# Kernel tuning notes

Hardware: AMD Instinct MI355X
Metric: run time of the kernel (lower is better)

The kernel has to match this reference:

```python
import math
import jax, jax.numpy as jnp
import numpy as np

VOCAB, D, H, L, DFF, MAXLEN, PAD = 32000, 512, 8, 6, 2048, 5000, 0
DK = D // H
EPS = 1e-5


def _positional_encoding(max_len, d_model):
    pos = np.arange(max_len, dtype=np.float32)[:, None]
    div = np.exp(np.arange(0, d_model, 2, dtype=np.float32) * (-math.log(10000.0) / d_model))
    pe = np.zeros((max_len, d_model), dtype=np.float32)
    pe[:, 0::2] = np.sin(pos * div)
    pe[:, 1::2] = np.cos(pos * div)
    return jnp.asarray(pe)


def setup_inputs() -> dict:
    key = jax.random.key(0)
    ks = jax.random.split(key, 16)
    B, S = 2, 2048
    src = jax.random.randint(ks[0], (B, S), 0, VOCAB)
    emb = jax.random.normal(ks[1], (VOCAB, D), jnp.float32) * (D ** -0.5)
    emb = emb.at[PAD].set(0.0)  # padding_idx row zeroed
    pe = _positional_encoding(MAXLEN, D)
    s = 0.02
    WQ = jax.random.normal(ks[2], (L, D, D), jnp.float32) * s
    WK = jax.random.normal(ks[3], (L, D, D), jnp.float32) * s
    WV = jax.random.normal(ks[4], (L, D, D), jnp.float32) * s
    WO = jax.random.normal(ks[5], (L, D, D), jnp.float32) * s
    W1 = jax.random.normal(ks[6], (L, D, DFF), jnp.float32) * s
    b1 = jnp.zeros((L, DFF), jnp.float32)
    W2 = jax.random.normal(ks[7], (L, DFF, D), jnp.float32) * s
    b2 = jnp.zeros((L, D), jnp.float32)
    ln1_s = jnp.ones((L, D), jnp.float32); ln1_b = jnp.zeros((L, D), jnp.float32)
    ln2_s = jnp.ones((L, D), jnp.float32); ln2_b = jnp.zeros((L, D), jnp.float32)
    fn_s = jnp.ones((D,), jnp.float32); fn_b = jnp.zeros((D,), jnp.float32)
    return dict(src=src, emb=emb, pe=pe, WQ=WQ, WK=WK, WV=WV, WO=WO,
                W1=W1, b1=b1, W2=W2, b2=b2, ln1_s=ln1_s, ln1_b=ln1_b,
                ln2_s=ln2_s, ln2_b=ln2_b, fn_s=fn_s, fn_b=fn_b)


def _layernorm(x, scale, bias):
    mu = jnp.mean(x, axis=-1, keepdims=True)
    var = jnp.mean(jnp.square(x - mu), axis=-1, keepdims=True)
    return (x - mu) * jax.lax.rsqrt(var + EPS) * scale + bias


def _encoder_forward(src, emb, pe, WQ, WK, WV, WO, W1, b1, W2, b2,
                     ln1_s, ln1_b, ln2_s, ln2_b, fn_s, fn_b):
    B, S = src.shape
    key_mask = (src != PAD)[:, None, None, :]  # [B,1,1,S] padding mask
    x = emb[src] * math.sqrt(D) + pe[:S]        # [B,S,D] (dropout=eval/off)
    for l in range(L):
        # --- pre-LN self-attention ---
        h = _layernorm(x, ln1_s[l], ln1_b[l])
        q = (h @ WQ[l]).reshape(B, S, H, DK).transpose(0, 2, 1, 3)
        k = (h @ WK[l]).reshape(B, S, H, DK).transpose(0, 2, 1, 3)
        v = (h @ WV[l]).reshape(B, S, H, DK).transpose(0, 2, 1, 3)
        scores = jnp.einsum('bhqd,bhkd->bhqk', q, k) / math.sqrt(DK)
        scores = jnp.where(key_mask, scores, -jnp.inf)
        w = jax.nn.softmax(scores, axis=-1)
        w = jnp.nan_to_num(w, nan=0.0)
        attn = jnp.einsum('bhqk,bhkd->bhqd', w, v)
        attn = attn.transpose(0, 2, 1, 3).reshape(B, S, D) @ WO[l]
        x = x + attn
        # --- pre-LN FFN ---
        h = _layernorm(x, ln2_s[l], ln2_b[l])
        h = jax.nn.relu(h @ W1[l] + b1[l]) @ W2[l] + b2[l]
        x = x + h
    return _layernorm(x, fn_s, fn_b)


def reference(src, emb, pe, WQ, WK, WV, WO, W1, b1, W2, b2,
              ln1_s, ln1_b, ln2_s, ln2_b, fn_s, fn_b):
    return _encoder_forward(src, emb, pe, WQ, WK, WV, WO, W1, b1, W2, b2,
                            ln1_s, ln1_b, ln2_s, ln2_b, fn_s, fn_b)
```

## Files before the change

kernel.cpp:

```cpp
#include <hip/hip_runtime.h>


typedef _Float16 f16;
typedef _Float16 f16x8 __attribute__((ext_vector_type(8)));
typedef _Float16 f16x4 __attribute__((ext_vector_type(4)));
typedef float    f32x4 __attribute__((ext_vector_type(4)));

#define MFMA16(a, b, c) __builtin_amdgcn_mfma_f32_16x16x32_f16((a), (b), (c), 0, 0, 0)
#define GLOAD_LDS16(GP, LP)                                        \
  __builtin_amdgcn_global_load_lds(                                \
      (const __attribute__((address_space(1))) void*)(GP),         \
      (__attribute__((address_space(3))) void*)(LP), 16, 0, 0)

__device__ inline float fast_exp2(float x) {
#if __has_builtin(__builtin_amdgcn_exp2f)
  return __builtin_amdgcn_exp2f(x);
#else
  return exp2f(x);
#endif
}

static constexpr int Dm  = 512;
static constexpr int Sx  = 2048;
static constexpr int NTOK = 4096;
static constexpr int DFFm = 2048;
static constexpr int Lc  = 6;

__global__ __launch_bounds__(256) void transpose_all(
    const float* __restrict__ WQ, const float* __restrict__ WK,
    const float* __restrict__ WV, const float* __restrict__ WO,
    const float* __restrict__ W1, const float* __restrict__ W2,
    f16* __restrict__ wqkv, f16* __restrict__ wtO,
    f16* __restrict__ wt1, f16* __restrict__ wt2)
{
  __shared__ float t[32][33];
  const size_t DD = (size_t)Dm * Dm;
  const size_t DQKV = (size_t)1536 * Dm;
  const size_t DF = (size_t)Dm * DFFm;
  int id = blockIdx.x;
  const float* src; f16* dst; int R, C, bx, by;
  if (id < 6144) {
    const int z = id >> 8, rem = id & 255;
    bx = rem & 15; by = rem >> 4;
    const int widx = z / 6, layer = z % 6;
    src = ((widx == 0) ? WQ : (widx == 1) ? WK : (widx == 2) ? WV : WO)
          + (size_t)layer * DD;
    dst = (widx < 3) ? wqkv + (size_t)layer * DQKV + (size_t)widx * 512 * Dm
                     : wtO + (size_t)layer * DD;
    R = 512; C = 512;
  } else if (id < 12288) {
    id -= 6144;
    const int layer = id >> 10, rem = id & 1023;
    bx = rem & 63; by = rem >> 6;
    src = W1 + (size_t)layer * DF;
    dst = wt1 + (size_t)layer * DF;
    R = 512; C = 2048;
  } else {
    id -= 12288;
    const int layer = id >> 10, rem = id & 1023;
    bx = rem & 15; by = rem >> 4;
    src = W2 + (size_t)layer * DF;
    dst = wt2 + (size_t)layer * DF;
    R = 2048; C = 512;
  }
  const int r0 = by * 32, c0 = bx * 32;
  const int tx = threadIdx.x, ty = threadIdx.y;
  #pragma unroll
  for (int i = 0; i < 4; i++)
    t[ty + i * 8][tx] = src[(size_t)(r0 + ty + i * 8) * C + c0 + tx];
  __syncthreads();
  #pragma unroll
  for (int i = 0; i < 4; i++)
    dst[(size_t)(c0 + ty + i * 8) * R + r0 + tx] = (f16)t[tx][ty + i * 8];
}

__global__ __launch_bounds__(256) void embed_k(
    const int* __restrict__ src, const float* __restrict__ emb,
    const float* __restrict__ pe, f16* __restrict__ x, float* __restrict__ mb)
{
  const int gid = blockIdx.x * 256 + threadIdx.x;
  const int token = gid >> 6;
  const int d0 = (gid & 63) << 3;
  const int s = token & (Sx - 1);
  const int tk = src[token];
  if ((gid & 63) == 0) mb[token] = (tk != 0) ? 0.f : -3.0e38f;
  const float* e = emb + (size_t)tk * Dm + d0;
  const float* p = pe + (size_t)s * Dm + d0;
  const float SC = 22.627416997969522f;
  f16x8 o;
  #pragma unroll
  for (int j = 0; j < 8; j++) o[j] = (f16)(e[j] * SC + p[j]);
  *(f16x8*)(x + (size_t)token * Dm + d0) = o;
}

template <typename OUT, int ADD, int BIAS, int WRITEX>
__global__ __launch_bounds__(256) void lnf_k(
    const f16* __restrict__ x, const f16* __restrict__ part,
    const f16* __restrict__ part2, const float* __restrict__ bias,
    const float* __restrict__ sc, const float* __restrict__ bi,
    OUT* __restrict__ out, f16* __restrict__ xout)
{
  const int row = blockIdx.x * 4 + (threadIdx.x >> 6);
  const int l = threadIdx.x & 63;
  f16x8 xv = *(const f16x8*)(x + (size_t)row * Dm + l * 8);
  float v[8];
  #pragma unroll
  for (int j = 0; j < 8; j++) v[j] = (float)xv[j];
  if constexpr (ADD >= 1) {
    f16x8 p = *(const f16x8*)(part + (size_t)row * Dm + l * 8);
    #pragma unroll
    for (int j = 0; j < 8; j++) v[j] += (float)p[j];
    if constexpr (ADD == 2) {
      f16x8 p2 = *(const f16x8*)(part2 + (size_t)row * Dm + l * 8);
      #pragma unroll
      for (int j = 0; j < 8; j++) v[j] += (float)p2[j];
    }
    if constexpr (BIAS) {
      float bb[8];
      *(float4*)&bb[0] = *(const float4*)(bias + l * 8);
      *(float4*)&bb[4] = *(const float4*)(bias + l * 8 + 4);
      #pragma unroll
      for (int j = 0; j < 8; j++) v[j] += bb[j];
    }
    if constexpr (WRITEX) {
      f16x8 xo;
      #pragma unroll
      for (int j = 0; j < 8; j++) xo[j] = (f16)v[j];
      *(f16x8*)(xout + (size_t)row * Dm + l * 8) = xo;
    }
  }
  float s = 0.f;
  #pragma unroll
  for (int j = 0; j < 8; j++) s += v[j];
  #pragma unroll
  for (int m = 1; m < 64; m <<= 1) s += __shfl_xor(s, m);
  const float mu = s * (1.0f / 512.0f);
  float qv = 0.f;
  #pragma unroll
  for (int j = 0; j < 8; j++) { float d = v[j] - mu; qv += d * d; }
  #pragma unroll
  for (int m = 1; m < 64; m <<= 1) qv += __shfl_xor(qv, m);
  const float inv = rsqrtf(qv * (1.0f / 512.0f) + 1e-5f);
  float scv[8], biv[8];
  *(float4*)&scv[0] = *(const float4*)(sc + l * 8);
  *(float4*)&scv[4] = *(const float4*)(sc + l * 8 + 4);
  *(float4*)&biv[0] = *(const float4*)(bi + l * 8);
  *(float4*)&biv[4] = *(const float4*)(bi + l * 8 + 4);
  if constexpr (sizeof(OUT) == 2) {
    f16x8 o;
    #pragma unroll
    for (int j = 0; j < 8; j++) o[j] = (f16)((v[j] - mu) * inv * scv[j] + biv[j]);
    *(f16x8*)((f16*)out + (size_t)row * Dm + l * 8) = o;
  } else {
    float o[8];
    #pragma unroll
    for (int j = 0; j < 8; j++) o[j] = (v[j] - mu) * inv * scv[j] + biv[j];
    float* po = (float*)out + (size_t)row * Dm + l * 8;
    *(float4*)po = *(float4*)&o[0];
    *(float4*)(po + 4) = *(float4*)&o[4];
  }
}

template <int BN, int MODE, int N, int K, int SK>
__global__ __launch_bounds__(256) void gemm_k(
    const f16* __restrict__ A, const f16* __restrict__ Bt,
    f16* __restrict__ O0, f16* __restrict__ O1, f16* __restrict__ O2,
    const float* __restrict__ bias)
{
  constexpr int BM = 128;
  constexpr int NF = (BN >= 32) ? BN / 32 : 1;
  constexpr int NBM = NTOK / BM;
  constexpr int NBN = N / BN;
  constexpr int NB = NBM * NBN * SK;
  __shared__ f16 lsA[2][BM * 64];
  __shared__ f16 lsB[2][BN * 64];
  const int tid = threadIdx.x;
  const int l = tid & 63, w = tid >> 6;
  const int lr = l & 15, lh = l >> 4;
  const int wm = w >> 1, wn = w & 1;
  const int bid = blockIdx.x;
  const int nid = (bid & 7) * (NB / 8) + (bid >> 3);
  const int ks = nid / (NBM * NBN);
  const int rr = nid % (NBM * NBN);
  const int bm = rr / NBN, bn = rr % NBN;

  constexpr int ACH = (BM * 64) / (256 * 8);
  constexpr int BCH = (BN * 64) / (256 * 8);
  const size_t rowA0 = (size_t)bm * BM;
  const size_t rowB0 = (size_t)bn * BN;
  const int k0 = ks * (K / SK);

  auto stage = [&](int kt, int pb) {
    #pragma unroll
    for (int i = 0; i < ACH; i++) {
      int c = i * 256 + tid, r = c >> 3, g = c & 7, gs = g ^ (r & 7);
      GLOAD_LDS16(A + (rowA0 + r) * K + k0 + kt * 64 + gs * 8, &lsA[pb][c * 8]);
    }
    #pragma unroll
    for (int i = 0; i < BCH; i++) {
      int c = i * 256 + tid, r = c >> 3, g = c & 7, gs = g ^ (r & 7);
      GLOAD_LDS16(Bt + (rowB0 + r) * K + k0 + kt * 64 + gs * 8, &lsB[pb][c * 8]);
    }
  };

  f32x4 acc[4][NF] = {};
  stage(0, 0);
  constexpr int NT = (K / SK) >> 6;
  for (int kt = 0; kt < NT; ++kt) {
    const int cur = kt & 1;
    __syncthreads();
    if (kt + 1 < NT) stage(kt + 1, cur ^ 1);
    #pragma unroll
    for (int s = 0; s < 2; s++) {
      const int gg = (s * 4 + lh) ^ (lr & 7);
      f16x8 af[4], bf[NF];
      #pragma unroll
      for (int mf = 0; mf < 4; mf++)
        af[mf] = *(const f16x8*)(&lsA[cur][(wm * 64 + mf * 16 + lr) * 64 + gg * 8]);
      #pragma unroll
      for (int nf = 0; nf < NF; nf++)
        bf[nf] = *(const f16x8*)(&lsB[cur][(wn * (BN / 2) + nf * 16 + lr) * 64 + gg * 8]);
      #pragma unroll
      for (int mf = 0; mf < 4; mf++)
        #pragma unroll
        for (int nf = 0; nf < NF; nf++)
          acc[mf][nf] = MFMA16(af[mf], bf[nf], acc[mf][nf]);
    }
  }

  #pragma unroll
  for (int mf = 0; mf < 4; mf++) {
    #pragma unroll
    for (int nf = 0; nf < NF; nf++) {
      const int token = bm * BM + wm * 64 + mf * 16 + lh * 4;
      const int ch = bn * BN + wn * (BN / 2) + nf * 16 + lr;
      if constexpr (MODE == 0) {
        const int part = ch >> 9;
        const int pch = ch & 511;
        if (part == 2) {
          f16x4 o;
          #pragma unroll
          for (int r = 0; r < 4; r++) o[r] = (f16)acc[mf][nf][r];
          const int bb = token >> 11, ss = token & (Sx - 1);
          const int scol = (ss & ~31) | (((ss >> 2) & 3) << 3) | (((ss >> 4) & 1) << 2);
          *(f16x4*)(O2 + ((size_t)((bb << 3) + (pch >> 6)) * 64 + (pch & 63)) * Sx + scol) = o;
        } else {
          f16* Oz = (part == 0) ? O0 : O1;
          #pragma unroll
          for (int r = 0; r < 4; r++)
            Oz[(size_t)(token + r) * Dm + pch] = (f16)acc[mf][nf][r];
        }
      } else if constexpr (MODE == 1) {
        #pragma unroll
        for (int r = 0; r < 4; r++)
          O0[(size_t)(token + r) * N + ch] = (f16)acc[mf][nf][r];
      } else if constexpr (MODE == 2) {
        #pragma unroll
        for (int r = 0; r < 4; r++) {
          float v = acc[mf][nf][r] + bias[ch];
          O0[(size_t)(token + r) * N + ch] = (f16)fmaxf(v, 0.f);
        }
      } else {
        f16* dst = O0 + (size_t)ks * NTOK * N;
        #pragma unroll
        for (int r = 0; r < 4; r++)
          dst[(size_t)(token + r) * N + ch] = (f16)acc[mf][nf][r];
      }
    }
  }
}

__global__ __launch_bounds__(512) void attn_k(
    const f16* __restrict__ q, const f16* __restrict__ kk,
    const f16* __restrict__ vt, const float* __restrict__ maskb,
    f16* __restrict__ out)
{
  __shared__ f16 lsK[2][2][64 * 64];
  __shared__ f16 lsV[2][2][64 * 64];
  const int tid = threadIdx.x;
  const int l = tid & 63, w = tid >> 6;
  const int lr = l & 15, lh = l >> 4;
  const int grp = w >> 2;
  const int t256 = tid & 255;
  const int bid = blockIdx.x;
  const int nid = ((bid & 7) << 6) + (bid >> 3);
  const int bh = nid >> 5;
  const int qt = nid & 31;
  const int b = bh >> 3, h = bh & 7;

  const _Float16 QS = (_Float16)0.18033688f;
  f16x8 qf[2];
  #pragma unroll
  for (int s = 0; s < 2; s++) {
    size_t row = (size_t)(b * Sx + qt * 64 + (w & 3) * 16 + lr);
    f16x8 t = *(const f16x8*)(q + row * Dm + h * 64 + s * 32 + lh * 8);
    qf[s] = t * QS;
  }

  const f16x8 ones = {(f16)1, (f16)1, (f16)1, (f16)1,
                      (f16)1, (f16)1, (f16)1, (f16)1};
  f32x4 oacc[4] = {};
  f32x4 sumacc = {};
  float mrun = -1e30f;

  auto stage = [&](int t, int pb) {
    #pragma unroll
    for (int i = 0; i < 2; i++) {
      int c = i * 256 + t256, r = c >> 3, g = c & 7, gs = g ^ (r & 7);
      GLOAD_LDS16(kk + (size_t)(b * Sx + t * 64 + r) * Dm + h * 64 + gs * 8,
                  &lsK[grp][pb][c * 8]);
      GLOAD_LDS16(vt + (size_t)(bh * 64 + r) * Sx + t * 64 + gs * 8,
                  &lsV[grp][pb][c * 8]);
    }
  };
  stage(grp * 16, 0);

  for (int i = 0; i < 16; ++i) {
    const int t = grp * 16 + i;
    const int cur = i & 1;
    __syncthreads();
    if (i < 15) stage(t + 1, cur ^ 1);

    f32x4 sacc[4];
    #pragma unroll
    for (int kf = 0; kf < 4; kf++)
      sacc[kf] = *(const f32x4*)(maskb + b * Sx + t * 64 + kf * 16 + lh * 4);
    __builtin_amdgcn_s_setprio(1);
    #pragma unroll
    for (int s = 0; s < 2; s++) {
      const int gk = (s * 4 + lh) ^ (lr & 7);
      #pragma unroll
      for (int kf = 0; kf < 4; kf++) {
        f16x8 a = *(const f16x8*)(&lsK[grp][cur][(kf * 16 + lr) * 64 + gk * 8]);
        sacc[kf] = MFMA16(a, qf[s], sacc[kf]);
      }
    }
    __builtin_amdgcn_s_setprio(0);

    float pmax;
    {
      float t0 = fmaxf(fmaxf(sacc[0][0], sacc[0][1]), sacc[0][2]);
      float t1 = fmaxf(fmaxf(sacc[0][3], sacc[1][0]), sacc[1][1]);
      float t2 = fmaxf(fmaxf(sacc[1][2], sacc[1][3]), sacc[2][0]);
      float t3 = fmaxf(fmaxf(sacc[2][1], sacc[2][2]), sacc[2][3]);
      float t4 = fmaxf(fmaxf(sacc[3][0], sacc[3][1]), sacc[3][2]);
      float u0 = fmaxf(fmaxf(t0, t1), sacc[3][3]);
      float u1 = fmaxf(fmaxf(t2, t3), t4);
      pmax = fmaxf(u0, u1);
    }
    pmax = fmaxf(pmax, __shfl_xor(pmax, 16));
    pmax = fmaxf(pmax, __shfl_xor(pmax, 32));
    if (!__all(pmax - mrun <= 8.0f)) {
      const float mnew = fmaxf(mrun, pmax);
      const float rs = fast_exp2(mrun - mnew);
      sumacc *= rs;
      #pragma unroll
      for (int mf = 0; mf < 4; mf++) oacc[mf] *= rs;
      mrun = mnew;
    }
    #pragma unroll
    for (int kf = 0; kf < 4; kf++)
      #pragma unroll
      for (int r = 0; r < 4; r++)
        sacc[kf][r] = fast_exp2(sacc[kf][r] - mrun);
    f16x8 pa[2];
    #pragma unroll
    for (int s = 0; s < 2; s++)
      #pragma unroll
      for (int jj = 0; jj < 8; jj++)
        pa[s][jj] = (f16)sacc[2 * s + (jj >> 2)][jj & 3];
    sumacc = MFMA16(ones, pa[0], sumacc);
    sumacc = MFMA16(ones, pa[1], sumacc);

    __builtin_amdgcn_s_setprio(1);
    #pragma unroll
    for (int s = 0; s < 2; s++) {
      const int gv = (4 * s + lh) ^ (lr & 7);
      #pragma unroll
      for (int mf = 0; mf < 4; mf++) {
        f16x8 vv = *(const f16x8*)(&lsV[grp][cur][(mf * 16 + lr) * 64 + gv * 8]);
        oacc[mf] = MFMA16(vv, pa[s], oacc[mf]);
      }
    }
    __builtin_amdgcn_s_setprio(0);
  }

  const float lrun = sumacc[0];
  __syncthreads();
  float* sO  = (float*)&lsK[0][0][0];
  float* sML = (float*)&lsV[0][0][0];
  const int wl = (w & 3) * 64 + l;
  if (grp == 1) {
    #pragma unroll
    for (int mf = 0; mf < 4; mf++)
      #pragma unroll
      for (int r = 0; r < 4; r++) sO[wl * 16 + mf * 4 + r] = oacc[mf][r];
    sML[wl * 2] = mrun;
    sML[wl * 2 + 1] = lrun;
  }
  __syncthreads();
  if (grp == 0) {
    const float m1 = sML[wl * 2], l1 = sML[wl * 2 + 1];
    const float mm = fmaxf(mrun, m1);
    const float s0 = fast_exp2(mrun - mm), s1 = fast_exp2(m1 - mm);
    const float inv = 1.f / (lrun * s0 + l1 * s1);
    size_t row = (size_t)(b * Sx + qt * 64 + (w & 3) * 16 + lr);
    #pragma unroll
    for (int mf = 0; mf < 4; mf++) {
      f16x4 o;
      #pragma unroll
      for (int r = 0; r < 4; r++)
        o[r] = (f16)((oacc[mf][r] * s0 + sO[wl * 16 + mf * 4 + r] * s1) * inv);
      *(f16x4*)(out + row * Dm + h * 64 + mf * 16 + lh * 4) = o;
    }
  }
}

extern "C" void kernel_launch(void* const* d_in, const int* in_sizes, int n_in,
                              void* d_out, int out_size, void* d_ws, size_t ws_size,
                              hipStream_t stream)
{
  (void)in_sizes; (void)n_in; (void)out_size; (void)ws_size;
  const int*   src  = (const int*)d_in[0];
  const float* emb  = (const float*)d_in[1];
  const float* pe   = (const float*)d_in[2];
  const float* WQ   = (const float*)d_in[3];
  const float* WK   = (const float*)d_in[4];
  const float* WV   = (const float*)d_in[5];
  const float* WO   = (const float*)d_in[6];
  const float* W1   = (const float*)d_in[7];
  const float* b1   = (const float*)d_in[8];
  const float* W2   = (const float*)d_in[9];
  const float* b2   = (const float*)d_in[10];
  const float* ln1s = (const float*)d_in[11];
  const float* ln1b = (const float*)d_in[12];
  const float* ln2s = (const float*)d_in[13];
  const float* ln2b = (const float*)d_in[14];
  const float* fns  = (const float*)d_in[15];
  const float* fnb  = (const float*)d_in[16];

  char* ws = (char*)d_ws;
  const size_t DD = (size_t)Dm * Dm;
  const size_t DQKV = (size_t)1536 * Dm;
  const size_t DF = (size_t)Dm * DFFm;
  f16* wqkv = (f16*)(ws);
  f16* wtO  = wqkv + Lc * DQKV;
  f16* wt1  = wtO + Lc * DD;
  f16* wt2  = wt1 + Lc * DF;
  f16* x    = wt2 + Lc * DF;
  f16* hbuf = x + (size_t)NTOK * Dm;
  f16* qb   = hbuf + (size_t)NTOK * Dm;
  f16* kb   = qb + (size_t)NTOK * Dm;
  f16* vtb  = kb + (size_t)NTOK * Dm;
  f16* attn = vtb + (size_t)NTOK * Dm;
  f16* aout = attn + (size_t)NTOK * Dm;
  f16* ff   = aout + (size_t)NTOK * Dm;
  f16* ffo  = ff + (size_t)NTOK * DFFm;
  float* maskb = (float*)(ffo + (size_t)2 * NTOK * Dm);

  transpose_all<<<18432, dim3(32, 8), 0, stream>>>(
      WQ, WK, WV, WO, W1, W2, wqkv, wtO, wt1, wt2);
  embed_k<<<1024, 256, 0, stream>>>(src, emb, pe, x, maskb);

  f16* ffo1 = ffo + (size_t)NTOK * Dm;
  for (int l = 0; l < Lc; l++) {
    const f16* wqkv_l = wqkv + (size_t)l * DQKV;
    const f16* wo = wtO + (size_t)l * DD;
    const f16* w1 = wt1 + (size_t)l * DF;
    const f16* w2 = wt2 + (size_t)l * DF;

    if (l == 0)
      lnf_k<f16, 0, 0, 0><<<1024, 256, 0, stream>>>(
          x, nullptr, nullptr, nullptr, ln1s, ln1b, hbuf, nullptr);
    else
      lnf_k<f16, 2, 1, 1><<<1024, 256, 0, stream>>>(
          x, ffo, ffo1, b2 + (size_t)(l - 1) * Dm, ln1s + l * Dm, ln1b + l * Dm,
          hbuf, x);
    gemm_k<64, 0, 1536, 512, 1><<<768, 256, 0, stream>>>(
        hbuf, wqkv_l, qb, kb, vtb, nullptr);
    attn_k<<<512, 512, 0, stream>>>(qb, kb, vtb, maskb, attn);
    gemm_k<32, 1, 512, 512, 1><<<512, 256, 0, stream>>>(
        attn, wo, aout, nullptr, nullptr, nullptr);
    lnf_k<f16, 1, 0, 1><<<1024, 256, 0, stream>>>(
        x, aout, nullptr, nullptr, ln2s + l * Dm, ln2b + l * Dm, hbuf, x);
    gemm_k<128, 2, 2048, 512, 1><<<512, 256, 0, stream>>>(
        hbuf, w1, ff, nullptr, nullptr, b1 + (size_t)l * DFFm);
    gemm_k<64, 3, 512, 2048, 2><<<512, 256, 0, stream>>>(
        ff, w2, ffo, nullptr, nullptr, nullptr);
  }

  lnf_k<float, 2, 1, 0><<<1024, 256, 0, stream>>>(
      x, ffo, ffo1, b2 + (size_t)(Lc - 1) * Dm, fns, fnb, (float*)d_out, nullptr);
}
```

Baseline: 600.1 us.

## Switch attention to 32x32 MFMA with four-way KV split per block

Rewrites the attention kernel to use 32x32x16 MFMA tiles instead of 16x16x32. Each block now runs four KV-split groups of two waves over 32-key tiles, where it used to run two groups of four waves over 64-key tiles. The row sum is now taken with a shuffle reduction instead of a ones-MFMA. The V-transpose write layout in the QKV projection epilogue is changed to match the new fragment ordering. The intent is fewer MFMA issues and more KV parallelism, in exchange for a four-way merge in LDS at the end and smaller tiles per iteration.

Result: slower. 637.1 us (+6.2%).

```diff
diff --git a/kernel.cpp b/kernel.cpp
--- a/kernel.cpp
+++ b/kernel.cpp
@@ -5,8 +5,10 @@
 typedef _Float16 f16x8 __attribute__((ext_vector_type(8)));
 typedef _Float16 f16x4 __attribute__((ext_vector_type(4)));
 typedef float    f32x4 __attribute__((ext_vector_type(4)));
+typedef float    f32x16 __attribute__((ext_vector_type(16)));
 
 #define MFMA16(a, b, c) __builtin_amdgcn_mfma_f32_16x16x32_f16((a), (b), (c), 0, 0, 0)
+#define MFMA32(a, b, c) __builtin_amdgcn_mfma_f32_32x32x16_f16((a), (b), (c), 0, 0, 0)
 #define GLOAD_LDS16(GP, LP)                                        \
   __builtin_amdgcn_global_load_lds(                                \
       (const __attribute__((address_space(1))) void*)(GP),         \
@@ -242,7 +244,8 @@
           #pragma unroll
           for (int r = 0; r < 4; r++) o[r] = (f16)acc[mf][nf][r];
           const int bb = token >> 11, ss = token & (Sx - 1);
-          const int scol = (ss & ~31) | (((ss >> 2) & 3) << 3) | (((ss >> 4) & 1) << 2);
+          const int scol = (ss & ~15) | (((ss >> 2) & 1) << 3)
+                         | (((ss >> 3) & 1) << 2) | (ss & 3);
           *(f16x4*)(O2 + ((size_t)((bb << 3) + (pch >> 6)) * 64 + (pch & 63)) * Sx + scol) = o;
         } else {
           f16* Oz = (part == 0) ? O0 : O1;
@@ -275,13 +278,14 @@
     const f16* __restrict__ vt, const float* __restrict__ maskb,
     f16* __restrict__ out)
 {
-  __shared__ f16 lsK[2][2][64 * 64];
-  __shared__ f16 lsV[2][2][64 * 64];
+  __shared__ f16 lds[32768];
+  f16* lsK = lds;
+  f16* lsV = lds + 16384;
   const int tid = threadIdx.x;
   const int l = tid & 63, w = tid >> 6;
-  const int lr = l & 15, lh = l >> 4;
-  const int grp = w >> 2;
-  const int t256 = tid & 255;
+  const int lq = l & 31, hi = l >> 5;
+  const int grp = w >> 1, wq = w & 1;
+  const int t128 = tid & 127;
   const int bid = blockIdx.x;
   const int nid = ((bid & 7) << 6) + (bid >> 3);
   const int bh = nid >> 5;
@@ -289,28 +293,34 @@
   const int b = bh >> 3, h = bh & 7;
 
   const _Float16 QS = (_Float16)0.18033688f;
-  f16x8 qf[2];
-  #pragma unroll
-  for (int s = 0; s < 2; s++) {
-    size_t row = (size_t)(b * Sx + qt * 64 + (w & 3) * 16 + lr);
-    f16x8 t = *(const f16x8*)(q + row * Dm + h * 64 + s * 32 + lh * 8);
-    qf[s] = t * QS;
-  }
-
-  const f16x8 ones = {(f16)1, (f16)1, (f16)1, (f16)1,
-                      (f16)1, (f16)1, (f16)1, (f16)1};
-  f32x4 oacc[4] = {};
-  f32x4 sumacc = {};
+  const size_t qrow = (size_t)(b * Sx + qt * 64 + wq * 32 + lq);
+  f16x8 qf[4];
+  #pragma unroll
+  for (int ks = 0; ks < 4; ks++) {
+    f16x8 t = *(const f16x8*)(q + qrow * Dm + h * 64 + ks * 16 + hi * 8);
+    qf[ks] = t * QS;
+  }
+
+  f32x16 oacc[2] = {};
   float mrun = -1e30f;
+  float lrun = 0.f;
 
   auto stage = [&](int t, int pb) {
+    f16* dK = lsK + (grp * 2 + pb) * 2048;
+    f16* dV = lsV + (grp * 2 + pb) * 2048;
     #pragma unroll
     for (int i = 0; i < 2; i++) {
-      int c = i * 256 + t256, r = c >> 3, g = c & 7, gs = g ^ (r & 7);
-      GLOAD_LDS16(kk + (size_t)(b * Sx + t * 64 + r) * Dm + h * 64 + gs * 8,
-                  &lsK[grp][pb][c * 8]);
-      GLOAD_LDS16(vt + (size_t)(bh * 64 + r) * Sx + t * 64 + gs * 8,
-                  &lsV[grp][pb][c * 8]);
+      int c = i * 128 + t128;
+      {
+        int r = c >> 3, g = c & 7, gs = g ^ (r & 7);
+        GLOAD_LDS16(kk + (size_t)(b * Sx + t * 32 + r) * Dm + h * 64 + gs * 8,
+                    dK + c * 8);
+      }
+      {
+        int dv = c >> 2, q2 = (c & 3) ^ (dv & 3);
+        GLOAD_LDS16(vt + (size_t)(bh * 64 + dv) * Sx + t * 32 + (q2 >> 1) * 16 + (q2 & 1) * 8,
+                    dV + c * 8);
+      }
     }
   };
   stage(grp * 16, 0);
@@ -320,99 +330,113 @@
     const int cur = i & 1;
     __syncthreads();
     if (i < 15) stage(t + 1, cur ^ 1);
-
-    f32x4 sacc[4];
-    #pragma unroll
-    for (int kf = 0; kf < 4; kf++)
-      sacc[kf] = *(const f32x4*)(maskb + b * Sx + t * 64 + kf * 16 + lh * 4);
+    const f16* cK = lsK + (grp * 2 + cur) * 2048;
+    const f16* cV = lsV + (grp * 2 + cur) * 2048;
+
+    f32x16 sacc;
+    #pragma unroll
+    for (int a = 0; a < 4; a++)
+      ((f32x4*)&sacc)[a] = *(const f32x4*)(maskb + b * Sx + t * 32 + 4 * hi + 8 * a);
     __builtin_amdgcn_s_setprio(1);
     #pragma unroll
-    for (int s = 0; s < 2; s++) {
-      const int gk = (s * 4 + lh) ^ (lr & 7);
-      #pragma unroll
-      for (int kf = 0; kf < 4; kf++) {
-        f16x8 a = *(const f16x8*)(&lsK[grp][cur][(kf * 16 + lr) * 64 + gk * 8]);
-        sacc[kf] = MFMA16(a, qf[s], sacc[kf]);
-      }
+    for (int ks = 0; ks < 4; ks++) {
+      f16x8 kf = *(const f16x8*)(cK + lq * 64 + (((ks * 2 + hi) ^ (lq & 7)) * 8));
+      sacc = MFMA32(kf, qf[ks], sacc);
     }
     __builtin_amdgcn_s_setprio(0);
 
     float pmax;
     {
-      float t0 = fmaxf(fmaxf(sacc[0][0], sacc[0][1]), sacc[0][2]);
-      float t1 = fmaxf(fmaxf(sacc[0][3], sacc[1][0]), sacc[1][1]);
-      float t2 = fmaxf(fmaxf(sacc[1][2], sacc[1][3]), sacc[2][0]);
-      float t3 = fmaxf(fmaxf(sacc[2][1], sacc[2][2]), sacc[2][3]);
-      float t4 = fmaxf(fmaxf(sacc[3][0], sacc[3][1]), sacc[3][2]);
-      float u0 = fmaxf(fmaxf(t0, t1), sacc[3][3]);
-      float u1 = fmaxf(fmaxf(t2, t3), t4);
-      pmax = fmaxf(u0, u1);
-    }
-    pmax = fmaxf(pmax, __shfl_xor(pmax, 16));
+      float t0 = fmaxf(fmaxf(sacc[0], sacc[1]), sacc[2]);
+      float t1 = fmaxf(fmaxf(sacc[3], sacc[4]), sacc[5]);
+      float t2 = fmaxf(fmaxf(sacc[6], sacc[7]), sacc[8]);
+      float t3 = fmaxf(fmaxf(sacc[9], sacc[10]), sacc[11]);
+      float t4 = fmaxf(fmaxf(sacc[12], sacc[13]), sacc[14]);
+      pmax = fmaxf(fmaxf(fmaxf(t0, t1), fmaxf(t2, t3)), fmaxf(t4, sacc[15]));
+    }
     pmax = fmaxf(pmax, __shfl_xor(pmax, 32));
     if (!__all(pmax - mrun <= 8.0f)) {
       const float mnew = fmaxf(mrun, pmax);
       const float rs = fast_exp2(mrun - mnew);
-      sumacc *= rs;
-      #pragma unroll
-      for (int mf = 0; mf < 4; mf++) oacc[mf] *= rs;
+      lrun *= rs;
+      oacc[0] *= rs;
+      oacc[1] *= rs;
       mrun = mnew;
     }
-    #pragma unroll
-    for (int kf = 0; kf < 4; kf++)
-      #pragma unroll
-      for (int r = 0; r < 4; r++)
-        sacc[kf][r] = fast_exp2(sacc[kf][r] - mrun);
-    f16x8 pa[2];
-    #pragma unroll
-    for (int s = 0; s < 2; s++)
-      #pragma unroll
-      for (int jj = 0; jj < 8; jj++)
-        pa[s][jj] = (f16)sacc[2 * s + (jj >> 2)][jj & 3];
-    sumacc = MFMA16(ones, pa[0], sumacc);
-    sumacc = MFMA16(ones, pa[1], sumacc);
+    float ps = 0.f;
+    #pragma unroll
+    for (int r = 0; r < 16; r++) {
+      float p = fast_exp2(sacc[r] - mrun);
+      sacc[r] = p;
+      ps += p;
+    }
+    ps += __shfl_xor(ps, 32);
+    lrun += ps;
+    f16x8 pb[2];
+    #pragma unroll
+    for (int g = 0; g < 2; g++)
+      #pragma unroll
+      for (int j = 0; j < 8; j++)
+        pb[g][j] = (f16)sacc[g * 8 + j];
 
     __builtin_amdgcn_s_setprio(1);
     #pragma unroll
-    for (int s = 0; s < 2; s++) {
-      const int gv = (4 * s + lh) ^ (lr & 7);
-      #pragma unroll
-      for (int mf = 0; mf < 4; mf++) {
-        f16x8 vv = *(const f16x8*)(&lsV[grp][cur][(mf * 16 + lr) * 64 + gv * 8]);
-        oacc[mf] = MFMA16(vv, pa[s], oacc[mf]);
+    for (int g = 0; g < 2; g++)
+      #pragma unroll
+      for (int mfv = 0; mfv < 2; mfv++) {
+        const int f = (mfv * 32 + lq) * 4 + ((2 * g + hi) ^ (lq & 3));
+        f16x8 vv = *(const f16x8*)(cV + f * 8);
+        oacc[mfv] = MFMA32(vv, pb[g], oacc[mfv]);
       }
-    }
     __builtin_amdgcn_s_setprio(0);
   }
 
-  const float lrun = sumacc[0];
   __syncthreads();
-  float* sO  = (float*)&lsK[0][0][0];
-  float* sML = (float*)&lsV[0][0][0];
-  const int wl = (w & 3) * 64 + l;
-  if (grp == 1) {
-    #pragma unroll
-    for (int mf = 0; mf < 4; mf++)
-      #pragma unroll
-      for (int r = 0; r < 4; r++) sO[wl * 16 + mf * 4 + r] = oacc[mf][r];
-    sML[wl * 2] = mrun;
-    sML[wl * 2 + 1] = lrun;
+  float* sO  = (float*)lds;
+  float* sML = (float*)lds + 12288;
+  const int slot = wq * 64 + l;
+  if (grp != 0) {
+    const int base = (grp - 1) * 128 + slot;
+    #pragma unroll
+    for (int mfv = 0; mfv < 2; mfv++)
+      #pragma unroll
+      for (int a = 0; a < 4; a++)
+        *(f32x4*)&sO[base * 32 + mfv * 16 + a * 4] = ((f32x4*)&oacc[mfv])[a];
+    sML[base * 2] = mrun;
+    sML[base * 2 + 1] = lrun;
   }
   __syncthreads();
   if (grp == 0) {
-    const float m1 = sML[wl * 2], l1 = sML[wl * 2 + 1];
-    const float mm = fmaxf(mrun, m1);
-    const float s0 = fast_exp2(mrun - mm), s1 = fast_exp2(m1 - mm);
-    const float inv = 1.f / (lrun * s0 + l1 * s1);
-    size_t row = (size_t)(b * Sx + qt * 64 + (w & 3) * 16 + lr);
-    #pragma unroll
-    for (int mf = 0; mf < 4; mf++) {
-      f16x4 o;
-      #pragma unroll
-      for (int r = 0; r < 4; r++)
-        o[r] = (f16)((oacc[mf][r] * s0 + sO[wl * 16 + mf * 4 + r] * s1) * inv);
-      *(f16x4*)(out + row * Dm + h * 64 + mf * 16 + lh * 4) = o;
-    }
+    float mg[3], lg[3];
+    #pragma unroll
+    for (int g = 0; g < 3; g++) {
+      mg[g] = sML[(g * 128 + slot) * 2];
+      lg[g] = sML[(g * 128 + slot) * 2 + 1];
+    }
+    const float mm = fmaxf(fmaxf(mrun, mg[0]), fmaxf(mg[1], mg[2]));
+    const float s0 = fast_exp2(mrun - mm);
+    float sg[3];
+    #pragma unroll
+    for (int g = 0; g < 3; g++) sg[g] = fast_exp2(mg[g] - mm);
+    const float inv = 1.f /
+        (lrun * s0 + lg[0] * sg[0] + lg[1] * sg[1] + lg[2] * sg[2]);
+    #pragma unroll
+    for (int mfv = 0; mfv < 2; mfv++)
+      #pragma unroll
+      for (int a = 0; a < 4; a++) {
+        f16x4 o;
+        #pragma unroll
+        for (int rr = 0; rr < 4; rr++) {
+          const int r = a * 4 + rr;
+          float v = oacc[mfv][r] * s0;
+          #pragma unroll
+          for (int g = 0; g < 3; g++)
+            v += sO[(g * 128 + slot) * 32 + mfv * 16 + r] * sg[g];
+          o[rr] = (f16)(v * inv);
+        }
+        const int dv = mfv * 32 + 4 * hi + 8 * a;
+        *(f16x4*)(out + qrow * Dm + h * 64 + dv) = o;
+      }
   }
 }
 
```
